# Kernel tuning notes

Hardware: AMD Instinct MI355X
Metric: run time of the kernel (lower is better)

## Reference

```python
import jax, jax.numpy as jnp
import numpy as np

N_NODES = 100_000
N_EDGES = 1_600_000
D = 128
BN_EPS = 1e-5
GIN_EPS = 0.0  # GINConv default eps, train_eps=False


def setup_inputs() -> dict:
    key = jax.random.key(0)
    ks = jax.random.split(key, 8)
    x = jax.random.normal(ks[0], (N_NODES, D), dtype=jnp.float32)
    edge_index = jax.random.randint(ks[1], (2, N_EDGES), 0, N_NODES, dtype=jnp.int64)
    s = 1.0 / np.sqrt(D)
    W1 = jax.random.uniform(ks[2], (D, D), jnp.float32, -s, s)
    b1 = jax.random.uniform(ks[3], (D,), jnp.float32, -s, s)
    W2 = jax.random.uniform(ks[4], (D, D), jnp.float32, -s, s)
    b2 = jax.random.uniform(ks[5], (D,), jnp.float32, -s, s)
    W3 = jax.random.uniform(ks[6], (D, D), jnp.float32, -s, s)
    g1 = jnp.ones((D,), jnp.float32)
    be1 = jnp.zeros((D,), jnp.float32)
    g2 = jnp.ones((D,), jnp.float32)
    be2 = jnp.zeros((D,), jnp.float32)
    return {"x": x, "edge_index": edge_index,
            "W1": W1, "b1": b1, "g1": g1, "be1": be1,
            "W2": W2, "b2": b2, "g2": g2, "be2": be2,
            "W3": W3}


def _batchnorm(h, gamma, beta):
    # training-mode BatchNorm1d over node dim with biased variance
    mean = jnp.mean(h, axis=0)
    var = jnp.mean(jnp.square(h - mean), axis=0)
    return (h - mean) * jax.lax.rsqrt(var + BN_EPS) * gamma + beta


def reference(x, edge_index, W1, b1, g1, be1, W2, b2, g2, be2, W3):
    src, dst = edge_index[0], edge_index[1]
    # GIN aggregation: (1+eps)*x_i + sum_{j->i} x_j  (scatter-add over edges)
    agg = jax.ops.segment_sum(x[src], dst, num_segments=N_NODES)
    h = (1.0 + GIN_EPS) * x + agg
    # MLP: Linear+BN+ReLU x2, then Linear (no bias)
    h = jax.nn.relu(_batchnorm(h @ W1.T + b1, g1, be1))
    h = jax.nn.relu(_batchnorm(h @ W2.T + b2, g2, be2))
    h = h @ W3.T
    # GINLayer final activation (bn=None)
    return jax.nn.relu(h)
```

## Files before the change

### kernel.cpp

```cpp
#include <hip/hip_runtime.h>

#define NN 100000
#define NE 1600000
#define DD 128
#define NCB 196
#define TILE 2048
#define NTILE 782
#define SREP 32

typedef __attribute__((ext_vector_type(8))) short bf16x8;
typedef __attribute__((ext_vector_type(4))) float f32x4;

union u4bf8 { uint4 u; bf16x8 v; };

__device__ __forceinline__ ushort f2bf(float f) {
    union { float f; uint i; } v; v.f = f;
    uint i = v.i;
    return (ushort)((i + 0x7fffu + ((i >> 16) & 1u)) >> 16);
}
__device__ __forceinline__ float bf2f(ushort u) {
    union { uint i; float f; } v; v.i = ((uint)u) << 16; return v.f;
}
__device__ __forceinline__ float blo(uint v) { return bf2f((ushort)(v & 0xffffu)); }
__device__ __forceinline__ float bhi(uint v) { return bf2f((ushort)(v >> 16)); }

__global__ __launch_bounds__(256) void k_xbh(const float* __restrict__ x,
                                             uint* __restrict__ xb,
                                             const int* __restrict__ ei,
                                             int* __restrict__ ghistP) {
    __shared__ int h[NCB];
    int t = threadIdx.x;
    if (t < NCB) h[t] = 0;
    __syncthreads();
    int base = blockIdx.x * TILE;
#pragma unroll
    for (int i = 0; i < 8; ++i) {
        int e = base + i * 256 + t;
        if (e < NE) atomicAdd(&h[ei[NE + e] >> 9], 1);
    }
    int gid = blockIdx.x * 256 + t;
#pragma unroll
    for (int i = 0; i < 8; ++i) {
        int item = i * (NTILE * 256) + gid;
        if (item < NN * 16) {
            int n = item >> 4, q = item & 15;
            const float* xp = x + (size_t)n * DD + q * 8;
            float4 a = *(const float4*)xp;
            float4 b = *(const float4*)(xp + 4);
            uint4 pk;
            pk.x = (uint)f2bf(a.x) | ((uint)f2bf(a.y) << 16);
            pk.y = (uint)f2bf(a.z) | ((uint)f2bf(a.w) << 16);
            pk.z = (uint)f2bf(b.x) | ((uint)f2bf(b.y) << 16);
            pk.w = (uint)f2bf(b.z) | ((uint)f2bf(b.w) << 16);
            *(uint4*)(xb + (size_t)n * 64 + q * 4) = pk;
        }
    }
    __syncthreads();
    if (t < NCB && h[t] > 0) atomicAdd(&ghistP[t * 16], h[t]);
}

__global__ void k_cscan(const int* __restrict__ ghistP, int* __restrict__ cb,
                        int* __restrict__ gcurP) {
    __shared__ int sh[NCB + 1];
    int t = threadIdx.x;
    if (t < NCB) sh[t] = ghistP[t * 16];
    __syncthreads();
    if (t == 0) {
        int run = 0;
        for (int i = 0; i < NCB; ++i) { int c = sh[i]; sh[i] = run; run += c; }
        sh[NCB] = run;
    }
    __syncthreads();
    if (t < NCB) { cb[t] = sh[t]; gcurP[t * 16] = sh[t]; }
    if (t == NCB) cb[NCB] = sh[NCB];
}

__global__ __launch_bounds__(256) void k_cscatter(const int* __restrict__ ei,
                                                  int* __restrict__ gcurP,
                                                  uint* __restrict__ buck) {
    __shared__ int h[NCB];
    __shared__ int tb[NCB];
    int t = threadIdx.x;
    if (t < NCB) h[t] = 0;
    __syncthreads();
    int base = blockIdx.x * TILE;
    uint vv[8]; int bb[8], rr[8];
#pragma unroll
    for (int i = 0; i < 8; ++i) {
        int e = base + i * 256 + t;
        bb[i] = -1;
        if (e < NE) {
            int s = ei[e], d = ei[NE + e];
            int b = d >> 9;
            bb[i] = b;
            vv[i] = (uint)s | ((uint)(d & 511) << 17);
            rr[i] = atomicAdd(&h[b], 1);
        }
    }
    __syncthreads();
    if (t < NCB && h[t] > 0) tb[t] = atomicAdd(&gcurP[t * 16], h[t]);
    __syncthreads();
#pragma unroll
    for (int i = 0; i < 8; ++i) {
        if (bb[i] >= 0) buck[tb[bb[i]] + rr[i]] = vv[i];
    }
}

__global__ __launch_bounds__(256) void k_fsort(const uint* __restrict__ buck,
                                               const int* __restrict__ cb,
                                               int* __restrict__ csr,
                                               int* __restrict__ rowp) {
    __shared__ int cnt[512];
    __shared__ int sd[256];
    int c = blockIdx.x, t = threadIdx.x;
    cnt[t] = 0; cnt[t + 256] = 0;
    __syncthreads();
    int s0 = cb[c], s1 = cb[c + 1];
    for (int i = s0 + t; i < s1; i += 256)
        atomicAdd(&cnt[(buck[i] >> 17) & 511], 1);
    __syncthreads();
    int p = cnt[2 * t], q = cnt[2 * t + 1];
    sd[t] = p + q;
    __syncthreads();
    for (int o = 1; o < 256; o <<= 1) {
        int u = (t >= o) ? sd[t - o] : 0;
        __syncthreads();
        sd[t] += u;
        __syncthreads();
    }
    int base = sd[t] - (p + q);
    rowp[c * 512 + 2 * t]     = s0 + base;
    rowp[c * 512 + 2 * t + 1] = s0 + base + p;
    __syncthreads();
    cnt[2 * t] = base;
    cnt[2 * t + 1] = base + p;
    __syncthreads();
    for (int i = s0 + t; i < s1; i += 256) {
        uint v = buck[i];
        int ld = (int)((v >> 17) & 511u);
        int pos = atomicAdd(&cnt[ld], 1);
        csr[s0 + pos] = (int)(v & 0x1FFFFu);
    }
}

#define B8(ACC0, ACC1, SJ, J)                                               \
    {                                                                       \
        int s0 = __shfl(SJ, J),     s1 = __shfl(SJ, J + 1);                 \
        int s2 = __shfl(SJ, J + 2), s3 = __shfl(SJ, J + 3);                 \
        int s4 = __shfl(SJ, J + 4), s5 = __shfl(SJ, J + 5);                 \
        int s6 = __shfl(SJ, J + 6), s7 = __shfl(SJ, J + 7);                 \
        uint v0 = xb[(size_t)s0 * 64 + lane], v1 = xb[(size_t)s1 * 64 + lane]; \
        uint v2 = xb[(size_t)s2 * 64 + lane], v3 = xb[(size_t)s3 * 64 + lane]; \
        uint v4 = xb[(size_t)s4 * 64 + lane], v5 = xb[(size_t)s5 * 64 + lane]; \
        uint v6 = xb[(size_t)s6 * 64 + lane], v7 = xb[(size_t)s7 * 64 + lane]; \
        ACC0 += blo(v0) + blo(v1) + blo(v2) + blo(v3)                       \
              + blo(v4) + blo(v5) + blo(v6) + blo(v7);                      \
        ACC1 += bhi(v0) + bhi(v1) + bhi(v2) + bhi(v3)                       \
              + bhi(v4) + bhi(v5) + bhi(v6) + bhi(v7);                      \
    }

__global__ __launch_bounds__(256) void k_gather(const uint* __restrict__ xb,
                                                const int* __restrict__ rowp,
                                                const int* __restrict__ csr,
                                                ushort* __restrict__ agg) {
    const int HALF = NN / 2;
    int wave = threadIdx.x >> 6, lane = threadIdx.x & 63;
    int w = blockIdx.x * 4 + wave;
    if (w >= HALF) return;
    int nA = w, nB = w + HALF;
    uint sA = xb[(size_t)nA * 64 + lane];
    uint sB = xb[(size_t)nB * 64 + lane];
    float a0 = blo(sA), a1 = bhi(sA);
    float b0 = blo(sB), b1 = bhi(sB);
    int iA = rowp[nA], eA = rowp[nA + 1];
    int iB = rowp[nB], eB = rowp[nB + 1];

    while (iA < eA || iB < eB) {
        int mA = eA - iA; if (mA > 64) mA = 64; if (mA < 0) mA = 0;
        int mB = eB - iB; if (mB > 64) mB = 64; if (mB < 0) mB = 0;
        int sjA = (lane < mA) ? csr[iA + lane] : 0;
        int sjB = (lane < mB) ? csr[iB + lane] : 0;
        int j = 0, k = 0;
        while (j + 8 <= mA && k + 8 <= mB) {
            int t0 = __shfl(sjA, j),     t1 = __shfl(sjA, j + 1);
            int t2 = __shfl(sjA, j + 2), t3 = __shfl(sjA, j + 3);
            int t4 = __shfl(sjA, j + 4), t5 = __shfl(sjA, j + 5);
            int t6 = __shfl(sjA, j + 6), t7 = __shfl(sjA, j + 7);
            int u0 = __shfl(sjB, k),     u1 = __shfl(sjB, k + 1);
            int u2 = __shfl(sjB, k + 2), u3 = __shfl(sjB, k + 3);
            int u4 = __shfl(sjB, k + 4), u5 = __shfl(sjB, k + 5);
            int u6 = __shfl(sjB, k + 6), u7 = __shfl(sjB, k + 7);
            uint vA0 = xb[(size_t)t0 * 64 + lane], vA1 = xb[(size_t)t1 * 64 + lane];
            uint vA2 = xb[(size_t)t2 * 64 + lane], vA3 = xb[(size_t)t3 * 64 + lane];
            uint vA4 = xb[(size_t)t4 * 64 + lane], vA5 = xb[(size_t)t5 * 64 + lane];
            uint vA6 = xb[(size_t)t6 * 64 + lane], vA7 = xb[(size_t)t7 * 64 + lane];
            uint vB0 = xb[(size_t)u0 * 64 + lane], vB1 = xb[(size_t)u1 * 64 + lane];
            uint vB2 = xb[(size_t)u2 * 64 + lane], vB3 = xb[(size_t)u3 * 64 + lane];
            uint vB4 = xb[(size_t)u4 * 64 + lane], vB5 = xb[(size_t)u5 * 64 + lane];
            uint vB6 = xb[(size_t)u6 * 64 + lane], vB7 = xb[(size_t)u7 * 64 + lane];
            a0 += blo(vA0) + blo(vA1) + blo(vA2) + blo(vA3)
                + blo(vA4) + blo(vA5) + blo(vA6) + blo(vA7);
            a1 += bhi(vA0) + bhi(vA1) + bhi(vA2) + bhi(vA3)
                + bhi(vA4) + bhi(vA5) + bhi(vA6) + bhi(vA7);
            b0 += blo(vB0) + blo(vB1) + blo(vB2) + blo(vB3)
                + blo(vB4) + blo(vB5) + blo(vB6) + blo(vB7);
            b1 += bhi(vB0) + bhi(vB1) + bhi(vB2) + bhi(vB3)
                + bhi(vB4) + bhi(vB5) + bhi(vB6) + bhi(vB7);
            j += 8; k += 8;
        }
        while (j + 8 <= mA) { B8(a0, a1, sjA, j) j += 8; }
        while (k + 8 <= mB) { B8(b0, b1, sjB, k) k += 8; }
        while (j < mA && k < mB) {
            int t = __shfl(sjA, j); int u = __shfl(sjB, k);
            uint vA = xb[(size_t)t * 64 + lane];
            uint vB = xb[(size_t)u * 64 + lane];
            a0 += blo(vA); a1 += bhi(vA);
            b0 += blo(vB); b1 += bhi(vB);
            ++j; ++k;
        }
        while (j < mA) {
            int t = __shfl(sjA, j++);
            uint vA = xb[(size_t)t * 64 + lane];
            a0 += blo(vA); a1 += bhi(vA);
        }
        while (k < mB) {
            int u = __shfl(sjB, k++);
            uint vB = xb[(size_t)u * 64 + lane];
            b0 += blo(vB); b1 += bhi(vB);
        }
        iA += mA; iB += mB;
    }

    uint pkA = (uint)f2bf(a0) | ((uint)f2bf(a1) << 16);
    uint pkB = (uint)f2bf(b0) | ((uint)f2bf(b1) << 16);
    ((uint*)(agg + (size_t)nA * DD))[lane] = pkA;
    ((uint*)(agg + (size_t)nB * DD))[lane] = pkB;
}

template <int MODE>
__global__ __launch_bounds__(256) void k_gemm(const ushort* __restrict__ Ain,
                                              const float* __restrict__ W,
                                              const float* __restrict__ bias,
                                              const float* __restrict__ statsIn,
                                              const float* __restrict__ g,
                                              const float* __restrict__ be,
                                              void* __restrict__ Outv,
                                              float* __restrict__ statsOut) {
    __shared__ ushort lw[DD * 136];
    __shared__ float red[2][4][DD];
    __shared__ float lac[2 * DD];

    int tid = threadIdx.x;
#pragma unroll
    for (int it = 0; it < 8; ++it) {
        int idx = (it * 256 + tid) * 8;
        int r = idx >> 7, k = idx & 127;
        float4 u0 = *(const float4*)(W + idx);
        float4 u1 = *(const float4*)(W + idx + 4);
        uint4 pk;
        pk.x = (uint)f2bf(u0.x) | ((uint)f2bf(u0.y) << 16);
        pk.y = (uint)f2bf(u0.z) | ((uint)f2bf(u0.w) << 16);
        pk.z = (uint)f2bf(u1.x) | ((uint)f2bf(u1.y) << 16);
        pk.w = (uint)f2bf(u1.z) | ((uint)f2bf(u1.w) << 16);
        *(uint4*)&lw[r * 136 + k] = pk;
    }
    if constexpr (MODE != 1) {
        if (tid < DD) {
            float S = 0.f, Q = 0.f;
#pragma unroll
            for (int r = 0; r < SREP; ++r) {
                S += statsIn[(r << 8) + tid];
                Q += statsIn[(r << 8) + DD + tid];
            }
            float inv = 1.f / (float)NN;
            float mean = S * inv;
            float var = Q * inv - mean * mean;
            float a = g[tid] * rsqrtf(var + 1e-5f);
            lac[tid] = a;
            lac[DD + tid] = be[tid] - mean * a;
        }
    }
    __syncthreads();

    int wave = tid >> 6, lane = tid & 63;
    int lm = lane & 15, quad = lane >> 4;
    int row0 = blockIdx.x * 64 + wave * 16;
    int arow = row0 + lm;
    int ar = (arow < NN) ? arow : 0;

    bf16x8 afrag[4];
#pragma unroll
    for (int kb = 0; kb < 4; ++kb) {
        int k0 = kb * 32 + quad * 8;
        const ushort* ap = Ain + (size_t)ar * DD + k0;
        u4bf8 u; u.u = *(const uint4*)ap;
        if constexpr (MODE == 1) {
            afrag[kb] = u.v;
        } else {
            uint pk[4] = {u.u.x, u.u.y, u.u.z, u.u.w};
            bf16x8 af;
#pragma unroll
            for (int jj = 0; jj < 4; ++jj) {
                int k = k0 + jj * 2;
                float v0 = blo(pk[jj]);
                float v1 = bhi(pk[jj]);
                v0 = fmaxf(fmaf(v0, lac[k], lac[DD + k]), 0.f);
                v1 = fmaxf(fmaf(v1, lac[k + 1], lac[DD + k + 1]), 0.f);
                af[jj * 2]     = (short)f2bf(v0);
                af[jj * 2 + 1] = (short)f2bf(v1);
            }
            afrag[kb] = af;
        }
    }

    f32x4 acc[8];
#pragma unroll
    for (int nt = 0; nt < 8; ++nt) {
        float bv = (MODE == 3) ? 0.f : bias[nt * 16 + lm];
        acc[nt] = (f32x4){bv, bv, bv, bv};
    }

#pragma unroll
    for (int kb = 0; kb < 4; ++kb) {
#pragma unroll
        for (int nt = 0; nt < 8; ++nt) {
            bf16x8 bfrag = *(const bf16x8*)&lw[(nt * 16 + lm) * 136 + kb * 32 + quad * 8];
            acc[nt] = __builtin_amdgcn_mfma_f32_16x16x32_bf16(afrag[kb], bfrag, acc[nt], 0, 0, 0);
        }
    }

    ushort* Out16 = (ushort*)Outv;
    float* Out32 = (float*)Outv;
    float csum[8], csq[8];
#pragma unroll
    for (int nt = 0; nt < 8; ++nt) {
        int col = nt * 16 + lm;
        float s = 0.f, q = 0.f;
#pragma unroll
        for (int r = 0; r < 4; ++r) {
            int row = row0 + quad * 4 + r;
            float v = acc[nt][r];
            if (MODE == 3) v = fmaxf(v, 0.f);
            if (row < NN) {
                if constexpr (MODE == 3) Out32[(size_t)row * DD + col] = v;
                else Out16[(size_t)row * DD + col] = f2bf(v);
                s += v;
                q += v * v;
            }
        }
        csum[nt] = s; csq[nt] = q;
    }

    if constexpr (MODE != 3) {
#pragma unroll
        for (int nt = 0; nt < 8; ++nt) {
            float s = csum[nt], q = csq[nt];
            s += __shfl_down(s, 16, 64); q += __shfl_down(q, 16, 64);
            s += __shfl_down(s, 32, 64); q += __shfl_down(q, 32, 64);
            if (quad == 0) {
                red[0][wave][nt * 16 + lm] = s;
                red[1][wave][nt * 16 + lm] = q;
            }
        }
        __syncthreads();
        if (tid < DD) {
            float S = red[0][0][tid] + red[0][1][tid] + red[0][2][tid] + red[0][3][tid];
            float Q = red[1][0][tid] + red[1][1][tid] + red[1][2][tid] + red[1][3][tid];
            int rep = (blockIdx.x & (SREP - 1)) << 8;
            atomicAdd(&statsOut[rep + tid], S);
            atomicAdd(&statsOut[rep + DD + tid], Q);
        }
    }
}

extern "C" void kernel_launch(void* const* d_in, const int* in_sizes, int n_in,
                              void* d_out, int out_size, void* d_ws, size_t ws_size,
                              hipStream_t stream) {
    const float* x   = (const float*)d_in[0];
    const int* ei    = (const int*)d_in[1];
    const float* W1  = (const float*)d_in[2];
    const float* b1  = (const float*)d_in[3];
    const float* g1  = (const float*)d_in[4];
    const float* be1 = (const float*)d_in[5];
    const float* W2  = (const float*)d_in[6];
    const float* b2  = (const float*)d_in[7];
    const float* g2  = (const float*)d_in[8];
    const float* be2 = (const float*)d_in[9];
    const float* W3  = (const float*)d_in[10];

    float* stats  = (float*)d_ws;
    float* stats2 = stats + SREP * 256;
    int* ghistP  = (int*)(stats + 2 * SREP * 256);
    int* cb      = ghistP + NCB * 16;
    int* gcurP   = cb + NCB + 4;
    int* rowp    = gcurP + NCB * 16;
    uint* buck   = (uint*)(rowp + NCB * 512 + 4);
    int* csr     = (int*)(buck + NE);
    ushort* agg  = (ushort*)(csr + NE);
    uint* xb     = (uint*)d_out;
    ushort* t1   = (ushort*)d_out + (size_t)NN * DD;
    ushort* t2   = agg;
    float* outp  = (float*)d_out;

    int gblk = (NN + 63) / 64;
    hipMemsetAsync(stats, 0, (2 * SREP * 256) * sizeof(float) + NCB * 16 * sizeof(int), stream);
    k_xbh<<<NTILE, 256, 0, stream>>>(x, xb, ei, ghistP);
    k_cscan<<<1, 256, 0, stream>>>(ghistP, cb, gcurP);
    k_cscatter<<<NTILE, 256, 0, stream>>>(ei, gcurP, buck);
    k_fsort<<<NCB, 256, 0, stream>>>(buck, cb, csr, rowp);
    k_gather<<<(NN / 2 + 3) / 4, 256, 0, stream>>>(xb, rowp, csr, agg);
    k_gemm<1><<<gblk, 256, 0, stream>>>(agg, W1, b1, nullptr, nullptr, nullptr, t1, stats);
    k_gemm<2><<<gblk, 256, 0, stream>>>(t1, W2, b2, stats, g1, be1, t2, stats2);
    k_gemm<3><<<gblk, 256, 0, stream>>>(t2, W3, nullptr, stats2, g2, be2, outp, nullptr);
}
```

Baseline: 310.2 us.

## Use finer destination buckets and pre-convert weights to padded bf16 once

Coarse destination buckets grow from 196 to 782 (128 nodes each), so the per-bucket fine sort runs on more, smaller blocks and uses less shared memory. The bucket prefix scan becomes a parallel 1024-thread scan. Weight matrices are converted to padded bf16 once in the first kernel, so each GEMM block does a plain copy into LDS instead of converting fp32 itself. SREP for the BN stat replicas is halved, which may add atomic contention in the stats accumulation.

```diff
diff --git a/kernel.cpp b/kernel.cpp
--- a/kernel.cpp
+++ b/kernel.cpp
@@ -3,10 +3,11 @@
 #define NN 100000
 #define NE 1600000
 #define DD 128
-#define NCB 196
+#define NCB 782
 #define TILE 2048
 #define NTILE 782
-#define SREP 32
+#define SREP 16
+#define WPAD 17408
 
 typedef __attribute__((ext_vector_type(8))) short bf16x8;
 typedef __attribute__((ext_vector_type(4))) float f32x4;
@@ -27,16 +28,20 @@
 __global__ __launch_bounds__(256) void k_xbh(const float* __restrict__ x,
                                              uint* __restrict__ xb,
                                              const int* __restrict__ ei,
-                                             int* __restrict__ ghistP) {
+                                             int* __restrict__ ghistP,
+                                             const float* __restrict__ W1,
+                                             const float* __restrict__ W2,
+                                             const float* __restrict__ W3,
+                                             ushort* __restrict__ Wbp) {
     __shared__ int h[NCB];
     int t = threadIdx.x;
-    if (t < NCB) h[t] = 0;
+    for (int i = t; i < NCB; i += 256) h[i] = 0;
     __syncthreads();
     int base = blockIdx.x * TILE;
 #pragma unroll
     for (int i = 0; i < 8; ++i) {
         int e = base + i * 256 + t;
-        if (e < NE) atomicAdd(&h[ei[NE + e] >> 9], 1);
+        if (e < NE) atomicAdd(&h[ei[NE + e] >> 7], 1);
     }
     int gid = blockIdx.x * 256 + t;
 #pragma unroll
@@ -55,24 +60,42 @@
             *(uint4*)(xb + (size_t)n * 64 + q * 4) = pk;
         }
     }
-    __syncthreads();
-    if (t < NCB && h[t] > 0) atomicAdd(&ghistP[t * 16], h[t]);
+    int c = gid;
+    if (c < 6144) {
+        int l = c >> 11;
+        int cc = c & 2047;
+        int r = cc >> 4, c8 = (cc & 15) * 8;
+        const float* Wl = (l == 0) ? W1 : (l == 1) ? W2 : W3;
+        const float* p = Wl + r * DD + c8;
+        float4 a = *(const float4*)p;
+        float4 b = *(const float4*)(p + 4);
+        uint4 pk;
+        pk.x = (uint)f2bf(a.x) | ((uint)f2bf(a.y) << 16);
+        pk.y = (uint)f2bf(a.z) | ((uint)f2bf(a.w) << 16);
+        pk.z = (uint)f2bf(b.x) | ((uint)f2bf(b.y) << 16);
+        pk.w = (uint)f2bf(b.z) | ((uint)f2bf(b.w) << 16);
+        *(uint4*)&Wbp[(size_t)l * WPAD + r * 136 + c8] = pk;
+    }
+    __syncthreads();
+    for (int i = t; i < NCB; i += 256)
+        if (h[i] > 0) atomicAdd(&ghistP[i * 16], h[i]);
 }
 
 __global__ void k_cscan(const int* __restrict__ ghistP, int* __restrict__ cb,
                         int* __restrict__ gcurP) {
-    __shared__ int sh[NCB + 1];
+    __shared__ int sh[1024];
     int t = threadIdx.x;
-    if (t < NCB) sh[t] = ghistP[t * 16];
-    __syncthreads();
-    if (t == 0) {
-        int run = 0;
-        for (int i = 0; i < NCB; ++i) { int c = sh[i]; sh[i] = run; run += c; }
-        sh[NCB] = run;
-    }
-    __syncthreads();
-    if (t < NCB) { cb[t] = sh[t]; gcurP[t * 16] = sh[t]; }
-    if (t == NCB) cb[NCB] = sh[NCB];
+    int my = (t < NCB) ? ghistP[t * 16] : 0;
+    sh[t] = my;
+    __syncthreads();
+    for (int o = 1; o < 1024; o <<= 1) {
+        int u = (t >= o) ? sh[t - o] : 0;
+        __syncthreads();
+        sh[t] += u;
+        __syncthreads();
+    }
+    if (t < NCB) { int ex = sh[t] - my; cb[t] = ex; gcurP[t * 16] = ex; }
+    if (t == NCB - 1) cb[NCB] = sh[t];
 }
 
 __global__ __launch_bounds__(256) void k_cscatter(const int* __restrict__ ei,
@@ -81,7 +104,7 @@
     __shared__ int h[NCB];
     __shared__ int tb[NCB];
     int t = threadIdx.x;
-    if (t < NCB) h[t] = 0;
+    for (int i = t; i < NCB; i += 256) h[i] = 0;
     __syncthreads();
     int base = blockIdx.x * TILE;
     uint vv[8]; int bb[8], rr[8];
@@ -91,14 +114,15 @@
         bb[i] = -1;
         if (e < NE) {
             int s = ei[e], d = ei[NE + e];
-            int b = d >> 9;
+            int b = d >> 7;
             bb[i] = b;
-            vv[i] = (uint)s | ((uint)(d & 511) << 17);
+            vv[i] = (uint)s | ((uint)(d & 127) << 17);
             rr[i] = atomicAdd(&h[b], 1);
         }
     }
     __syncthreads();
-    if (t < NCB && h[t] > 0) tb[t] = atomicAdd(&gcurP[t * 16], h[t]);
+    for (int i = t; i < NCB; i += 256)
+        if (h[i] > 0) tb[i] = atomicAdd(&gcurP[i * 16], h[i]);
     __syncthreads();
 #pragma unroll
     for (int i = 0; i < 8; ++i) {
@@ -110,34 +134,35 @@
                                                const int* __restrict__ cb,
                                                int* __restrict__ csr,
                                                int* __restrict__ rowp) {
-    __shared__ int cnt[512];
-    __shared__ int sd[256];
+    __shared__ int cnt[128];
+    __shared__ int sd[64];
     int c = blockIdx.x, t = threadIdx.x;
-    cnt[t] = 0; cnt[t + 256] = 0;
+    if (t < 128) cnt[t] = 0;
     __syncthreads();
     int s0 = cb[c], s1 = cb[c + 1];
     for (int i = s0 + t; i < s1; i += 256)
-        atomicAdd(&cnt[(buck[i] >> 17) & 511], 1);
-    __syncthreads();
-    int p = cnt[2 * t], q = cnt[2 * t + 1];
-    sd[t] = p + q;
-    __syncthreads();
-    for (int o = 1; o < 256; o <<= 1) {
-        int u = (t >= o) ? sd[t - o] : 0;
+        atomicAdd(&cnt[(buck[i] >> 17) & 127], 1);
+    __syncthreads();
+    int p = 0, q = 0;
+    if (t < 64) { p = cnt[2 * t]; q = cnt[2 * t + 1]; sd[t] = p + q; }
+    __syncthreads();
+    for (int o = 1; o < 64; o <<= 1) {
+        int u = (t >= o && t < 64) ? sd[t - o] : 0;
         __syncthreads();
-        sd[t] += u;
+        if (t < 64) sd[t] += u;
         __syncthreads();
     }
-    int base = sd[t] - (p + q);
-    rowp[c * 512 + 2 * t]     = s0 + base;
-    rowp[c * 512 + 2 * t + 1] = s0 + base + p;
-    __syncthreads();
-    cnt[2 * t] = base;
-    cnt[2 * t + 1] = base + p;
+    if (t < 64) {
+        int base = sd[t] - (p + q);
+        rowp[c * 128 + 2 * t]     = s0 + base;
+        rowp[c * 128 + 2 * t + 1] = s0 + base + p;
+        cnt[2 * t] = base;
+        cnt[2 * t + 1] = base + p;
+    }
     __syncthreads();
     for (int i = s0 + t; i < s1; i += 256) {
         uint v = buck[i];
-        int ld = (int)((v >> 17) & 511u);
+        int ld = (int)((v >> 17) & 127u);
         int pos = atomicAdd(&cnt[ld], 1);
         csr[s0 + pos] = (int)(v & 0x1FFFFu);
     }
@@ -239,30 +264,26 @@
 
 template <int MODE>
 __global__ __launch_bounds__(256) void k_gemm(const ushort* __restrict__ Ain,
-                                              const float* __restrict__ W,
+                                              const ushort* __restrict__ Wp,
                                               const float* __restrict__ bias,
                                               const float* __restrict__ statsIn,
                                               const float* __restrict__ g,
                                               const float* __restrict__ be,
                                               void* __restrict__ Outv,
                                               float* __restrict__ statsOut) {
-    __shared__ ushort lw[DD * 136];
+    __shared__ __align__(16) ushort lw[DD * 136];
     __shared__ float red[2][4][DD];
     __shared__ float lac[2 * DD];
 
     int tid = threadIdx.x;
 #pragma unroll
     for (int it = 0; it < 8; ++it) {
-        int idx = (it * 256 + tid) * 8;
-        int r = idx >> 7, k = idx & 127;
-        float4 u0 = *(const float4*)(W + idx);
-        float4 u1 = *(const float4*)(W + idx + 4);
-        uint4 pk;
-        pk.x = (uint)f2bf(u0.x) | ((uint)f2bf(u0.y) << 16);
-        pk.y = (uint)f2bf(u0.z) | ((uint)f2bf(u0.w) << 16);
-        pk.z = (uint)f2bf(u1.x) | ((uint)f2bf(u1.y) << 16);
-        pk.w = (uint)f2bf(u1.z) | ((uint)f2bf(u1.w) << 16);
-        *(uint4*)&lw[r * 136 + k] = pk;
+        int o8 = (it * 256 + tid) * 8;
+        *(uint4*)&lw[o8] = *(const uint4*)&Wp[o8];
+    }
+    if (tid < 128) {
+        int o8 = 16384 + tid * 8;
+        *(uint4*)&lw[o8] = *(const uint4*)&Wp[o8];
     }
     if constexpr (MODE != 1) {
         if (tid < DD) {
@@ -390,13 +411,14 @@
 
     float* stats  = (float*)d_ws;
     float* stats2 = stats + SREP * 256;
-    int* ghistP  = (int*)(stats + 2 * SREP * 256);
-    int* cb      = ghistP + NCB * 16;
-    int* gcurP   = cb + NCB + 4;
-    int* rowp    = gcurP + NCB * 16;
-    uint* buck   = (uint*)(rowp + NCB * 512 + 4);
-    int* csr     = (int*)(buck + NE);
-    ushort* agg  = (ushort*)(csr + NE);
+    int* ghistP   = (int*)(stats2 + SREP * 256);
+    ushort* Wbp   = (ushort*)(ghistP + NCB * 16);
+    int* cb       = (int*)(Wbp + 3 * WPAD);
+    int* gcurP    = cb + NCB + 4;
+    int* rowp     = gcurP + NCB * 16;
+    uint* buck    = (uint*)(rowp + NCB * 128 + 4);
+    int* csr      = (int*)(buck + NE);
+    ushort* agg   = (ushort*)(((uintptr_t)(csr + NE) + 15) & ~(uintptr_t)15);
     uint* xb     = (uint*)d_out;
     ushort* t1   = (ushort*)d_out + (size_t)NN * DD;
     ushort* t2   = agg;
@@ -404,12 +426,12 @@
 
     int gblk = (NN + 63) / 64;
     hipMemsetAsync(stats, 0, (2 * SREP * 256) * sizeof(float) + NCB * 16 * sizeof(int), stream);
-    k_xbh<<<NTILE, 256, 0, stream>>>(x, xb, ei, ghistP);
-    k_cscan<<<1, 256, 0, stream>>>(ghistP, cb, gcurP);
+    k_xbh<<<NTILE, 256, 0, stream>>>(x, xb, ei, ghistP, W1, W2, W3, Wbp);
+    k_cscan<<<1, 1024, 0, stream>>>(ghistP, cb, gcurP);
     k_cscatter<<<NTILE, 256, 0, stream>>>(ei, gcurP, buck);
     k_fsort<<<NCB, 256, 0, stream>>>(buck, cb, csr, rowp);
     k_gather<<<(NN / 2 + 3) / 4, 256, 0, stream>>>(xb, rowp, csr, agg);
-    k_gemm<1><<<gblk, 256, 0, stream>>>(agg, W1, b1, nullptr, nullptr, nullptr, t1, stats);
-    k_gemm<2><<<gblk, 256, 0, stream>>>(t1, W2, b2, stats, g1, be1, t2, stats2);
-    k_gemm<3><<<gblk, 256, 0, stream>>>(t2, W3, nullptr, stats2, g2, be2, outp, nullptr);
-}
+    k_gemm<1><<<gblk, 256, 0, stream>>>(agg, Wbp, b1, nullptr, nullptr, nullptr, t1, stats);
+    k_gemm<2><<<gblk, 256, 0, stream>>>(t1, Wbp + WPAD, b2, stats, g1, be1, t2, stats2);
+    k_gemm<3><<<gblk, 256, 0, stream>>>(t2, Wbp + 2 * WPAD, nullptr, stats2, g2, be2, outp, nullptr);
+}
```

New measurement: 327.2 us. 1.05x slower.
